# Optimization experiments

Measured on AMD Instinct MI355X. Metric: run time of the kernel, lower is better.

## Reference

```python
import jax, jax.numpy as jnp
import numpy as np

EPS = 1e-5  # BatchNorm1d default eps
DIMS = [(784, 1024), (1024, 1024), (1024, 1024), (1024, 10)]


def setup_inputs() -> dict:
    key = jax.random.key(0)
    ks = jax.random.split(key, 25)
    d = {"x": jax.random.normal(ks[0], (32768, 784), jnp.float32)}
    for i, (fi, fo) in enumerate(DIMS):
        j = i + 1
        base = 1 + 6 * i
        d[f"W{j}"] = jax.random.uniform(ks[base], (fo, fi), jnp.float32, -1.0, 1.0)
        d[f"b{j}"] = jnp.full((fo,), 0.01, jnp.float32)
        d[f"gamma{j}"] = jax.random.uniform(ks[base + 1], (fo,), jnp.float32, 0.5, 1.5)
        d[f"beta{j}"] = 0.1 * jax.random.normal(ks[base + 2], (fo,), jnp.float32)
        d[f"mean{j}"] = 0.1 * jax.random.normal(ks[base + 3], (fo,), jnp.float32)
        d[f"var{j}"] = jax.random.uniform(ks[base + 4], (fo,), jnp.float32, 0.5, 1.5)
    return d


def _bn(h, gamma, beta, mean, var):
    # inference-mode BatchNorm1d with running stats
    return gamma * (h - mean) * jax.lax.rsqrt(var + EPS) + beta


def reference(x,
              W1, b1, gamma1, beta1, mean1, var1,
              W2, b2, gamma2, beta2, mean2, var2,
              W3, b3, gamma3, beta3, mean3, var3,
              W4, b4, gamma4, beta4, mean4, var4):
    h = x.reshape(-1, 784)
    # layer 1: Quantizer(1) -> BinarizeLinear -> BN -> Hardtanh
    h = jnp.sign(h)
    h = h @ jnp.sign(W1).T + b1
    h = jnp.clip(_bn(h, gamma1, beta1, mean1, var1), -1.0, 1.0)
    # layer 2
    h = jnp.sign(h)
    h = h @ jnp.sign(W2).T + b2
    h = jnp.clip(_bn(h, gamma2, beta2, mean2, var2), -1.0, 1.0)
    # layer 3
    h = jnp.sign(h)
    h = h @ jnp.sign(W3).T + b3
    h = jnp.clip(_bn(h, gamma3, beta3, mean3, var3), -1.0, 1.0)
    # layer 4: Quantizer -> BinarizeLinear -> BN (no hardtanh)
    h = jnp.sign(h)
    h = h @ jnp.sign(W4).T + b4
    return _bn(h, gamma4, beta4, mean4, var4)
```

## Files before the change

### kernel.cpp

```cpp
#include <hip/hip_runtime.h>
#include <cstdint>
#include <climits>


typedef __attribute__((ext_vector_type(4))) int i32x4_t;

__device__ __forceinline__ void gload_lds16(const void* g, void* l) {
  __builtin_amdgcn_global_load_lds(
      (const __attribute__((address_space(1))) unsigned int*)g,
      (__attribute__((address_space(3))) unsigned int*)l, 16, 0, 0);
}

__device__ __forceinline__ int pack4(const float4 v) {
  int b0 = v.x > 0.f ? 1 : (v.x < 0.f ? -1 : 0);
  int b1 = v.y > 0.f ? 1 : (v.y < 0.f ? -1 : 0);
  int b2 = v.z > 0.f ? 1 : (v.z < 0.f ? -1 : 0);
  int b3 = v.w > 0.f ? 1 : (v.w < 0.f ? -1 : 0);
  return (b0 & 0xff) | ((b1 & 0xff) << 8) | ((b2 & 0xff) << 16) | (b3 << 24);
}


__global__ __launch_bounds__(256) void prep_mega_kernel(
    const float* __restrict__ x, int8_t* __restrict__ A0,
    const float* __restrict__ W1f, const float* __restrict__ W2f,
    const float* __restrict__ W3f, const float* __restrict__ W4f,
    int8_t* __restrict__ Wp1, int8_t* __restrict__ Wp2,
    int8_t* __restrict__ Wp3, int8_t* __restrict__ Wp4,
    const float* b1, const float* g1, const float* be1, const float* m1, const float* v1,
    const float* b2, const float* g2, const float* be2, const float* m2, const float* v2,
    const float* b3, const float* g3, const float* be3, const float* m3, const float* v3,
    const float* b4, const float* g4, const float* be4, const float* m4, const float* v4,
    int* __restrict__ T1, int* __restrict__ T2, int* __restrict__ T3,
    int8_t* __restrict__ S1, int8_t* __restrict__ S2, int8_t* __restrict__ S3,
    float* __restrict__ sc4, float* __restrict__ of4) {
  const int b = blockIdx.x;
  const int t = threadIdx.x;
  if (b < 32768) {
    const int col = t * 4;
    if (col < 784) {
      int packed = pack4(*(const float4*)(x + (size_t)b * 784 + col));
      *(int*)(A0 + (size_t)b * 832 + col) = packed;
    } else if (col < 832) {
      *(int*)(A0 + (size_t)b * 832 + col) = 0;
    }
  } else if (b < 35968) {
    const int b2i = b - 32768;
    const float* Wf; int8_t* Wp; int N, K, n, ost;
    if (b2i < 1024)      { Wf = W1f; Wp = Wp1; N = 1024; K = 784;  n = b2i;        ost = 832;  }
    else if (b2i < 2048) { Wf = W2f; Wp = Wp2; N = 1024; K = 1024; n = b2i - 1024; ost = 1024; }
    else if (b2i < 3072) { Wf = W3f; Wp = Wp3; N = 1024; K = 1024; n = b2i - 2048; ost = 1024; }
    else                 { Wf = W4f; Wp = Wp4; N = 10;   K = 1024; n = b2i - 3072; ost = 1024; }
    const int col = t * 4;
    if (col < ost) {
      int packed = 0;
      if (n < N && col + 3 < K)
        packed = pack4(*(const float4*)(Wf + (size_t)n * K + col));
      *(int*)(Wp + (size_t)n * ost + col) = packed;
    }
  } else {
    const int pb = b - 35968;
    if (pb < 12) {
      const int layer = pb >> 2;
      const int n = (pb & 3) * 256 + t;
      const float *bb, *gg, *be, *me, *va; int* T; int8_t* S;
      if (layer == 0)      { bb = b1; gg = g1; be = be1; me = m1; va = v1; T = T1; S = S1; }
      else if (layer == 1) { bb = b2; gg = g2; be = be2; me = m2; va = v2; T = T2; S = S2; }
      else                 { bb = b3; gg = g3; be = be3; me = m3; va = v3; T = T3; S = S3; }
      double g = (double)gg[n];
      double rs = 1.0 / sqrt((double)va[n] + 1e-5);
      int th; int8_t s;
      if (g > 0.0) {
        double tv = (double)me[n] - (double)bb[n] - (double)be[n] / (g * rs);
        tv = fmin(fmax(tv, -2.0e9), 2.0e9);
        th = (int)floor(tv) + 1; s = 1;
      } else if (g < 0.0) {
        double tv = (double)me[n] - (double)bb[n] - (double)be[n] / (g * rs);
        tv = fmin(fmax(tv, -2.0e9), 2.0e9);
        th = (int)ceil(tv); s = -1;
      } else {
        th = INT_MIN; s = (be[n] > 0.f) ? (int8_t)1 : (int8_t)-1;
      }
      T[n] = th; S[n] = s;
    } else if (t < 10) {
      double rs = 1.0 / sqrt((double)v4[t] + 1e-5);
      double sd = (double)g4[t] * rs;
      sc4[t] = (float)sd;
      of4[t] = (float)(sd * ((double)b4[t] - (double)m4[t]) + (double)be4[t]);
    }
  }
}

__global__ __launch_bounds__(512) void gemm_bnn256_kernel(
    const int8_t* __restrict__ A, const int8_t* __restrict__ W,
    int ldk, int nkt,
    const int* __restrict__ T, const int8_t* __restrict__ S,
    int8_t* __restrict__ Aout) {
  __shared__ i32x4_t smem[4096];
  int8_t* sm = (int8_t*)smem;
  const int tid = threadIdx.x;
  const int lane = tid & 63;
  const int w = tid >> 6;
  const int wm = w >> 2, wn = w & 3;

  const int bid = blockIdx.x;
  const int swz = (bid & 7) * 64 + (bid >> 3);
  const int row0 = (swz >> 2) * 256;
  const int col0 = (swz & 3) * 256;

  const int jj0 = tid, jj1 = tid + 512;
  const int r0 = jj0 >> 2, r1 = jj1 >> 2;
  const int s0 = (jj0 & 3) ^ ((r0 >> 1) & 3);
  const int s1 = (jj1 & 3) ^ ((r1 >> 1) & 3);
  const int8_t* aS0 = A + (size_t)(row0 + r0) * ldk + s0 * 16;
  const int8_t* aS1 = A + (size_t)(row0 + r1) * ldk + s1 * 16;
  const int8_t* bS0 = W + (size_t)(col0 + r0) * ldk + s0 * 16;
  const int8_t* bS1 = W + (size_t)(col0 + r1) * ldk + s1 * 16;
  const int dA0 = jj0 * 16, dA1 = jj1 * 16;
  const int dB0 = 16384 + jj0 * 16, dB1 = 16384 + jj1 * 16;

  int a_off[8], b_off[4];
#pragma unroll
  for (int m = 0; m < 8; ++m) {
    int ra = wm * 128 + m * 16 + (lane & 15);
    a_off[m] = ra * 64 + ((((lane >> 4) ^ (ra >> 1)) & 3) << 4);
  }
#pragma unroll
  for (int n = 0; n < 4; ++n) {
    int rb = wn * 64 + n * 16 + (lane & 15);
    b_off[n] = 16384 + rb * 64 + ((((lane >> 4) ^ (rb >> 1)) & 3) << 4);
  }

  i32x4_t acc[8][4];
#pragma unroll
  for (int m = 0; m < 8; ++m)
#pragma unroll
    for (int n = 0; n < 4; ++n) acc[m][n] = (i32x4_t){0, 0, 0, 0};

  gload_lds16(aS0, sm + dA0);
  gload_lds16(aS1, sm + dA1);
  gload_lds16(bS0, sm + dB0);
  gload_lds16(bS1, sm + dB1);

  for (int kt = 0; kt < nkt - 1; ++kt) {
    aS0 += 64; aS1 += 64; bS0 += 64; bS1 += 64;
    int8_t* smw = sm + (((kt + 1) & 1) << 15);
    gload_lds16(aS0, smw + dA0);
    gload_lds16(aS1, smw + dA1);
    gload_lds16(bS0, smw + dB0);
    gload_lds16(bS1, smw + dB1);
    asm volatile("s_waitcnt vmcnt(4)" ::: "memory");
    __builtin_amdgcn_s_barrier();
    const int8_t* smr = sm + ((kt & 1) << 15);
    i32x4_t av[8], bv[4];
#pragma unroll
    for (int i = 0; i < 8; ++i) av[i] = *(const i32x4_t*)(smr + a_off[i]);
#pragma unroll
    for (int i = 0; i < 4; ++i) bv[i] = *(const i32x4_t*)(smr + b_off[i]);
#pragma unroll
    for (int m = 0; m < 8; ++m)
#pragma unroll
      for (int n = 0; n < 4; ++n)
        acc[m][n] = __builtin_amdgcn_mfma_i32_16x16x64_i8(av[m], bv[n], acc[m][n], 0, 0, 0);
    __builtin_amdgcn_s_barrier();
  }
  asm volatile("s_waitcnt vmcnt(0)" ::: "memory");
  __builtin_amdgcn_s_barrier();
  {
    const int8_t* smr = sm + (((nkt - 1) & 1) << 15);
    i32x4_t av[8], bv[4];
#pragma unroll
    for (int i = 0; i < 8; ++i) av[i] = *(const i32x4_t*)(smr + a_off[i]);
#pragma unroll
    for (int i = 0; i < 4; ++i) bv[i] = *(const i32x4_t*)(smr + b_off[i]);
#pragma unroll
    for (int m = 0; m < 8; ++m)
#pragma unroll
      for (int n = 0; n < 4; ++n)
        acc[m][n] = __builtin_amdgcn_mfma_i32_16x16x64_i8(av[m], bv[n], acc[m][n], 0, 0, 0);
  }

#pragma unroll
  for (int n = 0; n < 4; ++n) {
    const int oc = col0 + wn * 64 + n * 16 + (lane & 15);
    const int tn = T[oc];
    const int8_t sn = S[oc];
#pragma unroll
    for (int m = 0; m < 8; ++m) {
      const int orb = row0 + wm * 128 + m * 16 + ((lane >> 4) << 2);
#pragma unroll
      for (int r = 0; r < 4; ++r) {
        int8_t v = (acc[m][n][r] >= tn) ? sn : (int8_t)(-sn);
        Aout[(size_t)(orb + r) * 1024 + oc] = v;
      }
    }
  }
}

__global__ __launch_bounds__(256) void gemm_final_kernel(
    const int8_t* __restrict__ A, const int8_t* __restrict__ W,
    int ldk, int nkt,
    const float* __restrict__ scale, const float* __restrict__ offs,
    float* __restrict__ out) {
  __shared__ i32x4_t smem[2048];
  int8_t* sm = (int8_t*)smem;
  const int tid = threadIdx.x;
  const int lane = tid & 63;
  const int w = tid >> 6;
  const int wrow = w >> 1, wcol = w & 1;
  const int row0 = blockIdx.x * 128;
  const int col0 = 0;

  const int jj0 = tid, jj1 = tid + 256;
  const int r0 = jj0 >> 2, r1 = jj1 >> 2;
  const int s0 = (jj0 & 3) ^ ((r0 >> 1) & 3);
  const int s1 = (jj1 & 3) ^ ((r1 >> 1) & 3);
  const int8_t* aS0 = A + (size_t)(row0 + r0) * ldk + s0 * 16;
  const int8_t* aS1 = A + (size_t)(row0 + r1) * ldk + s1 * 16;
  const int8_t* bS0 = W + (size_t)(col0 + r0) * ldk + s0 * 16;
  const int8_t* bS1 = W + (size_t)(col0 + r1) * ldk + s1 * 16;
  const int dA0 = jj0 * 16, dA1 = jj1 * 16;
  const int dB0 = 8192 + jj0 * 16, dB1 = 8192 + jj1 * 16;

  int a_off[4], b_off[4];
#pragma unroll
  for (int i = 0; i < 4; ++i) {
    int ra = wrow * 64 + i * 16 + (lane & 15);
    a_off[i] = ra * 64 + ((((lane >> 4) ^ (ra >> 1)) & 3) << 4);
    int rb = wcol * 64 + i * 16 + (lane & 15);
    b_off[i] = 8192 + rb * 64 + ((((lane >> 4) ^ (rb >> 1)) & 3) << 4);
  }

  i32x4_t acc[4][4];
#pragma unroll
  for (int m = 0; m < 4; ++m)
#pragma unroll
    for (int n = 0; n < 4; ++n) acc[m][n] = (i32x4_t){0, 0, 0, 0};

  gload_lds16(aS0, sm + dA0);
  gload_lds16(aS1, sm + dA1);
  gload_lds16(bS0, sm + dB0);
  gload_lds16(bS1, sm + dB1);

  for (int kt = 0; kt < nkt - 1; ++kt) {
    aS0 += 64; aS1 += 64; bS0 += 64; bS1 += 64;
    int8_t* smw = sm + (((kt + 1) & 1) << 14);
    gload_lds16(aS0, smw + dA0);
    gload_lds16(aS1, smw + dA1);
    gload_lds16(bS0, smw + dB0);
    gload_lds16(bS1, smw + dB1);
    asm volatile("s_waitcnt vmcnt(4)" ::: "memory");
    __builtin_amdgcn_s_barrier();
    const int8_t* smr = sm + ((kt & 1) << 14);
    i32x4_t av[4], bv[4];
#pragma unroll
    for (int i = 0; i < 4; ++i) av[i] = *(const i32x4_t*)(smr + a_off[i]);
#pragma unroll
    for (int i = 0; i < 4; ++i) bv[i] = *(const i32x4_t*)(smr + b_off[i]);
#pragma unroll
    for (int m = 0; m < 4; ++m)
#pragma unroll
      for (int n = 0; n < 4; ++n)
        acc[m][n] = __builtin_amdgcn_mfma_i32_16x16x64_i8(av[m], bv[n], acc[m][n], 0, 0, 0);
    __builtin_amdgcn_s_barrier();
  }
  asm volatile("s_waitcnt vmcnt(0)" ::: "memory");
  __builtin_amdgcn_s_barrier();
  {
    const int8_t* smr = sm + (((nkt - 1) & 1) << 14);
    i32x4_t av[4], bv[4];
#pragma unroll
    for (int i = 0; i < 4; ++i) av[i] = *(const i32x4_t*)(smr + a_off[i]);
#pragma unroll
    for (int i = 0; i < 4; ++i) bv[i] = *(const i32x4_t*)(smr + b_off[i]);
#pragma unroll
    for (int m = 0; m < 4; ++m)
#pragma unroll
      for (int n = 0; n < 4; ++n)
        acc[m][n] = __builtin_amdgcn_mfma_i32_16x16x64_i8(av[m], bv[n], acc[m][n], 0, 0, 0);
  }

#pragma unroll
  for (int n = 0; n < 4; ++n) {
    const int oc = col0 + wcol * 64 + n * 16 + (lane & 15);
    if (oc < 10) {
      const float sc = scale[oc], of = offs[oc];
#pragma unroll
      for (int m = 0; m < 4; ++m) {
        const int orb = row0 + wrow * 64 + m * 16 + ((lane >> 4) << 2);
#pragma unroll
        for (int r = 0; r < 4; ++r)
          out[(size_t)(orb + r) * 10 + oc] = sc * (float)acc[m][n][r] + of;
      }
    }
  }
}


#define A0_STRIDE 28

__global__ __launch_bounds__(256) void pack_w_kernel(
    const float* __restrict__ W, uint32_t* __restrict__ Wp,
    int nout, int K, int wstride) {
  int idx = blockIdx.x * blockDim.x + threadIdx.x;
  if (idx >= nout * wstride) return;
  int n = idx / wstride;
  int wi = idx - n * wstride;
  const float* wr = W + (size_t)n * K;
  uint32_t word = 0;
  int base = wi * 32;
  for (int i = 0; i < 32; ++i) {
    int c = base + i;
    if (c < K && wr[c] > 0.f) word |= (1u << i);
  }
  Wp[idx] = word;
}

__global__ __launch_bounds__(256) void prep_thr_kernel(
    const float* __restrict__ b, const float* __restrict__ gamma,
    const float* __restrict__ beta, const float* __restrict__ mean,
    const float* __restrict__ var, int K, int N,
    int* __restrict__ thr, uint32_t* __restrict__ flipm) {
  int n = blockIdx.x * blockDim.x + threadIdx.x;
  if (n >= N) return;
  double g = (double)gamma[n];
  double rs = 1.0 / sqrt((double)var[n] + 1e-5);
  int th;
  if (g != 0.0) {
    double t = (double)mean[n] - (double)b[n] - (double)beta[n] / (g * rs);
    double pt = ((double)K - t) * 0.5;
    th = (g > 0.0) ? (int)ceil(pt) : ((int)floor(pt) + 1);
  } else {
    th = (beta[n] > 0.f) ? (K + 2) : -1;
  }
  thr[n] = th;
  if ((n & 31) == 0) {
    uint32_t m = 0;
    for (int i = 0; i < 32 && (n + i) < N; ++i)
      if (gamma[n + i] < 0.f) m |= (1u << i);
    flipm[n >> 5] = m;
  }
}

__global__ __launch_bounds__(64) void prep_out_kernel(
    const float* __restrict__ b, const float* __restrict__ gamma,
    const float* __restrict__ beta, const float* __restrict__ mean,
    const float* __restrict__ var, int N,
    float* __restrict__ s, float* __restrict__ o) {
  int n = threadIdx.x;
  if (n >= N) return;
  double rs = 1.0 / sqrt((double)var[n] + 1e-5);
  double sd = (double)gamma[n] * rs;
  s[n] = (float)sd;
  o[n] = (float)(sd * ((double)b[n] - (double)mean[n]) + (double)beta[n]);
}

__global__ __launch_bounds__(256) void pack_a_kernel(
    const float* __restrict__ x, uint32_t* __restrict__ A0) {
  int gt = blockIdx.x * blockDim.x + threadIdx.x;
  int wv = gt >> 6;
  int lane = gt & 63;
  int row = wv / 13;
  int seg = wv - row * 13;
  int col = (seg << 6) + lane;
  bool pred = (col < 784) && (x[(size_t)row * 784 + col] > 0.f);
  unsigned long long m = __ballot(pred);
  int widx = seg * 2;
  if (lane == 0)
    A0[(size_t)row * A0_STRIDE + widx] = (uint32_t)m;
  else if (lane == 1 && widx + 1 < 25)
    A0[(size_t)row * A0_STRIDE + widx + 1] = (uint32_t)(m >> 32);
}

__device__ __forceinline__ void layer1024(
    uint32_t a[32], const uint32_t* __restrict__ Wp,
    const int* __restrict__ thr, const uint32_t* __restrict__ fm,
    uint32_t* lds, int lane, int w) {
  const int nb = w * 128;
  uint32_t word = 0;
#pragma unroll 2
  for (int ni = 0; ni < 128; ++ni) {
    const int n = nb + ni;
    const uint32_t* __restrict__ wp = Wp + n * 32;
    uint32_t p0 = 0, p1 = 0, p2 = 0, p3 = 0;
#pragma unroll
    for (int k = 0; k < 32; k += 4) {
      p0 += __popc(a[k + 0] ^ wp[k + 0]);
      p1 += __popc(a[k + 1] ^ wp[k + 1]);
      p2 += __popc(a[k + 2] ^ wp[k + 2]);
      p3 += __popc(a[k + 3] ^ wp[k + 3]);
    }
    int p = (int)(p0 + p1 + p2 + p3);
    word |= ((p < thr[n]) ? 1u : 0u) << (ni & 31);
    if ((ni & 31) == 31) {
      lds[lane * 33 + (n >> 5)] = word ^ fm[n >> 5];
      word = 0;
    }
  }
  __syncthreads();
#pragma unroll
  for (int k = 0; k < 32; ++k) a[k] = lds[lane * 33 + k];
  __syncthreads();
}

__global__ __launch_bounds__(512, 4) void fused_kernel(
    const uint32_t* __restrict__ A0,
    const uint32_t* __restrict__ Wp1, const int* __restrict__ thr1, const uint32_t* __restrict__ fm1,
    const uint32_t* __restrict__ Wp2, const int* __restrict__ thr2, const uint32_t* __restrict__ fm2,
    const uint32_t* __restrict__ Wp3, const int* __restrict__ thr3, const uint32_t* __restrict__ fm3,
    const uint32_t* __restrict__ Wp4, const float* __restrict__ s4, const float* __restrict__ o4,
    float* __restrict__ out) {
  __shared__ uint32_t lds[64 * 33];
  const int lane = threadIdx.x & 63;
  const int w = __builtin_amdgcn_readfirstlane((int)(threadIdx.x >> 6));
  const int row = blockIdx.x * 64 + lane;

  uint32_t a[32];
  {
    const uint4* A4 = (const uint4*)(A0 + (size_t)row * A0_STRIDE);
#pragma unroll
    for (int i = 0; i < 7; ++i) {
      uint4 q = A4[i];
      a[4 * i + 0] = q.x; a[4 * i + 1] = q.y; a[4 * i + 2] = q.z; a[4 * i + 3] = q.w;
    }
  }
  {
    const int nb = w * 128;
    uint32_t word = 0;
#pragma unroll 2
    for (int ni = 0; ni < 128; ++ni) {
      const int n = nb + ni;
      const uint32_t* __restrict__ wp = Wp1 + n * A0_STRIDE;
      uint32_t p0 = 0, p1 = 0, p2 = 0, p3 = 0;
#pragma unroll
      for (int k = 0; k < 24; k += 4) {
        p0 += __popc(a[k + 0] ^ wp[k + 0]);
        p1 += __popc(a[k + 1] ^ wp[k + 1]);
        p2 += __popc(a[k + 2] ^ wp[k + 2]);
        p3 += __popc(a[k + 3] ^ wp[k + 3]);
      }
      p0 += __popc(a[24] ^ wp[24]);
      int p = (int)(p0 + p1 + p2 + p3);
      word |= ((p < thr1[n]) ? 1u : 0u) << (ni & 31);
      if ((ni & 31) == 31) {
        lds[lane * 33 + (n >> 5)] = word ^ fm1[n >> 5];
        word = 0;
      }
    }
    __syncthreads();
#pragma unroll
    for (int k = 0; k < 32; ++k) a[k] = lds[lane * 33 + k];
    __syncthreads();
  }
  layer1024(a, Wp2, thr2, fm2, lds, lane, w);
  layer1024(a, Wp3, thr3, fm3, lds, lane, w);
  for (int j = w; j < 10; j += 8) {
    const uint32_t* __restrict__ wp = Wp4 + j * 32;
    uint32_t p0 = 0, p1 = 0, p2 = 0, p3 = 0;
#pragma unroll
    for (int k = 0; k < 32; k += 4) {
      p0 += __popc(a[k + 0] ^ wp[k + 0]);
      p1 += __popc(a[k + 1] ^ wp[k + 1]);
      p2 += __popc(a[k + 2] ^ wp[k + 2]);
      p3 += __popc(a[k + 3] ^ wp[k + 3]);
    }
    float dotf = 1024.f - 2.f * (float)(p0 + p1 + p2 + p3);
    out[(size_t)row * 10 + j] = s4[j] * dotf + o4[j];
  }
}

extern "C" void kernel_launch(void* const* d_in, const int* in_sizes, int n_in,
                              void* d_out, int out_size, void* d_ws, size_t ws_size,
                              hipStream_t stream) {
  const float* x   = (const float*)d_in[0];
  const float* W1  = (const float*)d_in[1];
  const float* b1  = (const float*)d_in[2];
  const float* g1  = (const float*)d_in[3];
  const float* be1 = (const float*)d_in[4];
  const float* m1  = (const float*)d_in[5];
  const float* v1  = (const float*)d_in[6];
  const float* W2  = (const float*)d_in[7];
  const float* b2  = (const float*)d_in[8];
  const float* g2  = (const float*)d_in[9];
  const float* be2 = (const float*)d_in[10];
  const float* m2  = (const float*)d_in[11];
  const float* v2  = (const float*)d_in[12];
  const float* W3  = (const float*)d_in[13];
  const float* b3  = (const float*)d_in[14];
  const float* g3  = (const float*)d_in[15];
  const float* be3 = (const float*)d_in[16];
  const float* m3  = (const float*)d_in[17];
  const float* v3  = (const float*)d_in[18];
  const float* W4  = (const float*)d_in[19];
  const float* b4  = (const float*)d_in[20];
  const float* g4  = (const float*)d_in[21];
  const float* be4 = (const float*)d_in[22];
  const float* m4  = (const float*)d_in[23];
  const float* v4  = (const float*)d_in[24];
  float* outp = (float*)d_out;
  (void)in_sizes; (void)n_in; (void)out_size;

  uint8_t* ws = (uint8_t*)d_ws;
  const size_t NEED = 100ULL << 20;

  if (ws_size >= NEED) {
    size_t off = 0;
    int8_t* A0  = (int8_t*)(ws + off); off += (size_t)32768 * 832;
    int8_t* Bp1 = (int8_t*)(ws + off); off += (size_t)32768 * 1024;
    int8_t* Bp2 = (int8_t*)(ws + off); off += (size_t)32768 * 1024;
    int8_t* Wp1 = (int8_t*)(ws + off); off += (size_t)1024 * 832;
    int8_t* Wp2 = (int8_t*)(ws + off); off += (size_t)1024 * 1024;
    int8_t* Wp3 = (int8_t*)(ws + off); off += (size_t)1024 * 1024;
    int8_t* Wp4 = (int8_t*)(ws + off); off += (size_t)128 * 1024;
    int* T1     = (int*)(ws + off);    off += 4096;
    int* T2     = (int*)(ws + off);    off += 4096;
    int* T3     = (int*)(ws + off);    off += 4096;
    int8_t* S1  = (int8_t*)(ws + off); off += 1024;
    int8_t* S2  = (int8_t*)(ws + off); off += 1024;
    int8_t* S3  = (int8_t*)(ws + off); off += 1024;
    float* sc4  = (float*)(ws + off);  off += 512;
    float* of4  = (float*)(ws + off);  off += 512;

    prep_mega_kernel<<<35981, 256, 0, stream>>>(
        x, A0, W1, W2, W3, W4, Wp1, Wp2, Wp3, Wp4,
        b1, g1, be1, m1, v1, b2, g2, be2, m2, v2,
        b3, g3, be3, m3, v3, b4, g4, be4, m4, v4,
        T1, T2, T3, S1, S2, S3, sc4, of4);

    gemm_bnn256_kernel<<<512, 512, 0, stream>>>(A0, Wp1, 832, 13, T1, S1, Bp1);
    gemm_bnn256_kernel<<<512, 512, 0, stream>>>(Bp1, Wp2, 1024, 16, T2, S2, Bp2);
    gemm_bnn256_kernel<<<512, 512, 0, stream>>>(Bp2, Wp3, 1024, 16, T3, S3, Bp1);
    gemm_final_kernel<<<256, 256, 0, stream>>>(Bp1, Wp4, 1024, 16, sc4, of4, outp);
  } else {
    size_t off = 0;
    uint32_t* A0  = (uint32_t*)(ws + off); off += (size_t)32768 * A0_STRIDE * 4;
    uint32_t* Wp1 = (uint32_t*)(ws + off); off += (size_t)1024 * A0_STRIDE * 4;
    uint32_t* Wp2 = (uint32_t*)(ws + off); off += (size_t)1024 * 32 * 4;
    uint32_t* Wp3 = (uint32_t*)(ws + off); off += (size_t)1024 * 32 * 4;
    uint32_t* Wp4 = (uint32_t*)(ws + off); off += 4096;
    int* thr1     = (int*)(ws + off);      off += 4096;
    int* thr2     = (int*)(ws + off);      off += 4096;
    int* thr3     = (int*)(ws + off);      off += 4096;
    uint32_t* fm1 = (uint32_t*)(ws + off); off += 128;
    uint32_t* fm2 = (uint32_t*)(ws + off); off += 128;
    uint32_t* fm3 = (uint32_t*)(ws + off); off += 128;
    float* s4o    = (float*)(ws + off);    off += 64;
    float* o4o    = (float*)(ws + off);    off += 64;

    pack_w_kernel<<<(1024 * A0_STRIDE + 255) / 256, 256, 0, stream>>>(W1, Wp1, 1024, 784, A0_STRIDE);
    pack_w_kernel<<<(1024 * 32 + 255) / 256, 256, 0, stream>>>(W2, Wp2, 1024, 1024, 32);
    pack_w_kernel<<<(1024 * 32 + 255) / 256, 256, 0, stream>>>(W3, Wp3, 1024, 1024, 32);
    pack_w_kernel<<<(10 * 32 + 255) / 256, 256, 0, stream>>>(W4, Wp4, 10, 1024, 32);
    prep_thr_kernel<<<4, 256, 0, stream>>>(b1, g1, be1, m1, v1, 784, 1024, thr1, fm1);
    prep_thr_kernel<<<4, 256, 0, stream>>>(b2, g2, be2, m2, v2, 1024, 1024, thr2, fm2);
    prep_thr_kernel<<<4, 256, 0, stream>>>(b3, g3, be3, m3, v3, 1024, 1024, thr3, fm3);
    prep_out_kernel<<<1, 64, 0, stream>>>(b4, g4, be4, m4, v4, 10, s4o, o4o);
    pack_a_kernel<<<(32768 * 13) / 4, 256, 0, stream>>>(x, A0);
    fused_kernel<<<512, 512, 0, stream>>>(A0, Wp1, thr1, fm1, Wp2, thr2, fm2,
                                          Wp3, thr3, fm3, Wp4, s4o, o4o, outp);
  }
}
```

Before: 324.0 us.

## Split hidden-layer GEMM k-loop into two half-phases with staggered prefetch and setprio

Restructures the main binary GEMM k-loop so each tile is computed in two halves of A rows. The A prefetch for the next stage is issued before the first half and the B prefetch after a mid barrier, which spreads global-to-LDS traffic across the iteration. The MFMA blocks are wrapped in s_setprio raises, and the peeled last iteration is folded into the loop. It adds an extra barrier per iteration, and the barrier builtins become asm volatile with a memory clobber.

```diff
diff --git a/kernel.cpp b/kernel.cpp
--- a/kernel.cpp
+++ b/kernel.cpp
@@ -141,42 +141,56 @@
   gload_lds16(bS0, sm + dB0);
   gload_lds16(bS1, sm + dB1);
 
-  for (int kt = 0; kt < nkt - 1; ++kt) {
-    aS0 += 64; aS1 += 64; bS0 += 64; bS1 += 64;
-    int8_t* smw = sm + (((kt + 1) & 1) << 15);
-    gload_lds16(aS0, smw + dA0);
-    gload_lds16(aS1, smw + dA1);
-    gload_lds16(bS0, smw + dB0);
-    gload_lds16(bS1, smw + dB1);
-    asm volatile("s_waitcnt vmcnt(4)" ::: "memory");
-    __builtin_amdgcn_s_barrier();
-    const int8_t* smr = sm + ((kt & 1) << 15);
-    i32x4_t av[8], bv[4];
-#pragma unroll
-    for (int i = 0; i < 8; ++i) av[i] = *(const i32x4_t*)(smr + a_off[i]);
-#pragma unroll
-    for (int i = 0; i < 4; ++i) bv[i] = *(const i32x4_t*)(smr + b_off[i]);
-#pragma unroll
-    for (int m = 0; m < 8; ++m)
-#pragma unroll
-      for (int n = 0; n < 4; ++n)
-        acc[m][n] = __builtin_amdgcn_mfma_i32_16x16x64_i8(av[m], bv[n], acc[m][n], 0, 0, 0);
-    __builtin_amdgcn_s_barrier();
-  }
-  asm volatile("s_waitcnt vmcnt(0)" ::: "memory");
-  __builtin_amdgcn_s_barrier();
-  {
-    const int8_t* smr = sm + (((nkt - 1) & 1) << 15);
-    i32x4_t av[8], bv[4];
-#pragma unroll
-    for (int i = 0; i < 8; ++i) av[i] = *(const i32x4_t*)(smr + a_off[i]);
-#pragma unroll
-    for (int i = 0; i < 4; ++i) bv[i] = *(const i32x4_t*)(smr + b_off[i]);
-#pragma unroll
-    for (int m = 0; m < 8; ++m)
-#pragma unroll
-      for (int n = 0; n < 4; ++n)
-        acc[m][n] = __builtin_amdgcn_mfma_i32_16x16x64_i8(av[m], bv[n], acc[m][n], 0, 0, 0);
+  for (int kt = 0; kt < nkt; ++kt) {
+    const int nxt = kt + 1;
+    int8_t* const bufw = sm + ((nxt & 1) << 15);
+    const int8_t* const bufr = sm + ((kt & 1) << 15);
+
+    if (nxt < nkt) {
+      aS0 += 64; aS1 += 64;
+      gload_lds16(aS0, bufw + dA0);
+      gload_lds16(aS1, bufw + dA1);
+      asm volatile("s_waitcnt vmcnt(2)" ::: "memory");
+    } else {
+      asm volatile("s_waitcnt vmcnt(0)" ::: "memory");
+    }
+    asm volatile("s_barrier" ::: "memory");
+
+    i32x4_t bv[4];
+#pragma unroll
+    for (int i = 0; i < 4; ++i) bv[i] = *(const i32x4_t*)(bufr + b_off[i]);
+    {
+      i32x4_t av[4];
+#pragma unroll
+      for (int i = 0; i < 4; ++i) av[i] = *(const i32x4_t*)(bufr + a_off[i]);
+      __builtin_amdgcn_s_setprio(1);
+#pragma unroll
+      for (int m = 0; m < 4; ++m)
+#pragma unroll
+        for (int n = 0; n < 4; ++n)
+          acc[m][n] = __builtin_amdgcn_mfma_i32_16x16x64_i8(av[m], bv[n], acc[m][n], 0, 0, 0);
+      __builtin_amdgcn_s_setprio(0);
+    }
+    asm volatile("s_barrier" ::: "memory");
+
+    if (nxt < nkt) {
+      bS0 += 64; bS1 += 64;
+      gload_lds16(bS0, bufw + dB0);
+      gload_lds16(bS1, bufw + dB1);
+    }
+    {
+      i32x4_t av[4];
+#pragma unroll
+      for (int i = 0; i < 4; ++i) av[i] = *(const i32x4_t*)(bufr + a_off[4 + i]);
+      __builtin_amdgcn_s_setprio(1);
+#pragma unroll
+      for (int m = 0; m < 4; ++m)
+#pragma unroll
+        for (int n = 0; n < 4; ++n)
+          acc[4 + m][n] = __builtin_amdgcn_mfma_i32_16x16x64_i8(av[m], bv[n], acc[4 + m][n], 0, 0, 0);
+      __builtin_amdgcn_s_setprio(0);
+    }
+    asm volatile("s_barrier" ::: "memory");
   }
 
 #pragma unroll
@@ -249,7 +263,7 @@
     gload_lds16(bS0, smw + dB0);
     gload_lds16(bS1, smw + dB1);
     asm volatile("s_waitcnt vmcnt(4)" ::: "memory");
-    __builtin_amdgcn_s_barrier();
+    asm volatile("s_barrier" ::: "memory");
     const int8_t* smr = sm + ((kt & 1) << 14);
     i32x4_t av[4], bv[4];
 #pragma unroll
@@ -261,10 +275,10 @@
 #pragma unroll
       for (int n = 0; n < 4; ++n)
         acc[m][n] = __builtin_amdgcn_mfma_i32_16x16x64_i8(av[m], bv[n], acc[m][n], 0, 0, 0);
-    __builtin_amdgcn_s_barrier();
+    asm volatile("s_barrier" ::: "memory");
   }
   asm volatile("s_waitcnt vmcnt(0)" ::: "memory");
-  __builtin_amdgcn_s_barrier();
+  asm volatile("s_barrier" ::: "memory");
   {
     const int8_t* smr = sm + (((nkt - 1) & 1) << 14);
     i32x4_t av[4], bv[4];
```

Result: no change. 328.8 us (+1.5%).
